# Optimization experiments

Measured on AMD Instinct MI355X. Metric: run time of the kernel, lower is better.

The kernel has to match this reference:

```python
import jax, jax.numpy as jnp
import numpy as np

N_NODES = 50000
N_EDGES = 800000
IN_CH, HID_CH, OUT_CH = 128, 256, 128


def _glorot(key, shape):
    fan_in, fan_out = shape[1], shape[0]
    lim = float(np.sqrt(6.0 / (fan_in + fan_out)))
    return jax.random.uniform(key, shape, jnp.float32, -lim, lim)


def setup_inputs() -> dict:
    key = jax.random.key(0)
    ks = jax.random.split(key, 8)
    x = jax.random.normal(ks[0], (N_NODES, IN_CH), jnp.float32)
    edge_index = jax.random.randint(ks[1], (2, N_EDGES), 0, N_NODES, jnp.int64)
    return {
        "x": x,
        "edge_index": edge_index,
        # layer 1: SAGEConv(128 -> 256): lin_l (with bias) on aggregated, lin_r (no bias) on root
        "W1l": _glorot(ks[2], (HID_CH, IN_CH)),
        "b1l": jnp.zeros((HID_CH,), jnp.float32),
        "W1r": _glorot(ks[3], (HID_CH, IN_CH)),
        # layer 2: SAGEConv(256 -> 128)
        "W2l": _glorot(ks[4], (OUT_CH, HID_CH)),
        "b2l": jnp.zeros((OUT_CH,), jnp.float32),
        "W2r": _glorot(ks[5], (OUT_CH, HID_CH)),
    }


def _sage_conv(x, src, dst, Wl, bl, Wr, n_nodes):
    # mean-aggregate neighbor (source) features at destination nodes
    msg = x[src]                                                   # [E, C] gather
    agg = jax.ops.segment_sum(msg, dst, num_segments=n_nodes)      # [N, C]
    deg = jax.ops.segment_sum(jnp.ones((src.shape[0],), x.dtype), dst,
                              num_segments=n_nodes)                # [N]
    mean = agg / jnp.maximum(deg, 1.0)[:, None]                    # zero-degree -> 0
    return mean @ Wl.T + bl + x @ Wr.T


def reference(x, edge_index, W1l, b1l, W1r, W2l, b2l, W2r):
    src, dst = edge_index[0], edge_index[1]
    n = x.shape[0]
    h = _sage_conv(x, src, dst, W1l, b1l, W1r, n)
    h = jax.nn.relu(h)  # dropout is identity in eval mode
    out = _sage_conv(h, src, dst, W2l, b2l, W2r, n)
    return out
```

## Files before the change

### kernel.cpp

```cpp
#include <hip/hip_runtime.h>

#define N_NODES 50000
#define IN_CH   128
#define HID_CH  256
#define OUT_CH  128

#define NB    196
#define NWG   256
#define NBNW  (NB * NWG)

#define XBLK  3125
#define WBLK  64

typedef __attribute__((ext_vector_type(8))) short bf16x8;
typedef __attribute__((ext_vector_type(4))) float f32x4;
typedef __attribute__((ext_vector_type(2))) float f32x2;

__device__ __forceinline__ unsigned short f32_bf16_rne(float f) {
    unsigned u = __float_as_uint(f);
    unsigned r = u + 0x7fff + ((u >> 16) & 1);
    return (unsigned short)(r >> 16);
}

__device__ __forceinline__ void cvt8_io(const float* __restrict__ inp,
                                        unsigned short* __restrict__ outp)
{
    const float4* p = reinterpret_cast<const float4*>(inp);
    float4 a = p[0], b = p[1];
    alignas(16) unsigned short t[8] = {
        f32_bf16_rne(a.x), f32_bf16_rne(a.y), f32_bf16_rne(a.z), f32_bf16_rne(a.w),
        f32_bf16_rne(b.x), f32_bf16_rne(b.y), f32_bf16_rne(b.z), f32_bf16_rne(b.w)};
    *reinterpret_cast<int4*>(outp) = *reinterpret_cast<const int4*>(t);
}

__global__ __launch_bounds__(256) void prep_kernel(
    const int* __restrict__ src, const int* __restrict__ dst,
    int* __restrict__ counts, int E, int chunk,
    const float* __restrict__ x, unsigned short* __restrict__ A1,
    unsigned char* __restrict__ xb8,
    const float* __restrict__ W1l, const float* __restrict__ W1r,
    const float* __restrict__ W2l, const float* __restrict__ W2r,
    unsigned short* __restrict__ B1, unsigned short* __restrict__ W2cat)
{
    const int b = blockIdx.x;
    if (b < NWG) {
        __shared__ int h[NB];
        for (int i = threadIdx.x; i < NB; i += 256) h[i] = 0;
        __syncthreads();
        const int e0 = b * chunk;
        const int e1 = min(e0 + chunk, E);
        for (int e = e0 + threadIdx.x; e < e1; e += 256) {
            int s = src[e], d = dst[e];
            if ((unsigned)s < (unsigned)N_NODES && (unsigned)d < (unsigned)N_NODES)
                atomicAdd(&h[d >> 8], 1);
        }
        __syncthreads();
        for (int i = threadIdx.x; i < NB; i += 256)
            counts[i * NWG + b] = h[i];
    } else if (b < NWG + XBLK) {
        size_t j = (size_t)(b - NWG) * 256 + threadIdx.x;
        const float4* p = reinterpret_cast<const float4*>(x) + 2 * j;
        float4 a = p[0], bb = p[1];
        alignas(16) unsigned short t[8] = {
            f32_bf16_rne(a.x),  f32_bf16_rne(a.y),  f32_bf16_rne(a.z),  f32_bf16_rne(a.w),
            f32_bf16_rne(bb.x), f32_bf16_rne(bb.y), f32_bf16_rne(bb.z), f32_bf16_rne(bb.w)};
        const size_t node = j >> 4, chunk16 = j & 15;
        *reinterpret_cast<int4*>(A1 + node * 256 + 128 + chunk16 * 8) =
            *reinterpret_cast<const int4*>(t);
        unsigned u0 = __builtin_amdgcn_cvt_pk_fp8_f32(a.x, a.y, 0, false);
        u0 = __builtin_amdgcn_cvt_pk_fp8_f32(a.z, a.w, u0, true);
        unsigned u1 = __builtin_amdgcn_cvt_pk_fp8_f32(bb.x, bb.y, 0, false);
        u1 = __builtin_amdgcn_cvt_pk_fp8_f32(bb.z, bb.w, u1, true);
        uint2 uv; uv.x = u0; uv.y = u1;
        *reinterpret_cast<uint2*>(xb8 + 8 * j) = uv;
    } else {
        int idx = (b - NWG - XBLK) * 256 + threadIdx.x;
        int seg = idx >> 12, j = idx & 4095;
        if (seg == 0) {
            int row = j >> 4, cb = (j & 15) * 8;
            cvt8_io(W1l + (size_t)j * 8, B1 + (size_t)row * 256 + cb);
        } else if (seg == 1) {
            int row = j >> 4, cb = (j & 15) * 8;
            cvt8_io(W1r + (size_t)j * 8, B1 + (size_t)row * 256 + 128 + cb);
        } else if (seg == 2) {
            int row = j >> 5, cb = (j & 31) * 8;
            cvt8_io(W2l + (size_t)j * 8, W2cat + (size_t)row * 256 + cb);
        } else {
            int row = j >> 5, cb = (j & 31) * 8;
            cvt8_io(W2r + (size_t)j * 8, W2cat + (size_t)(128 + row) * 256 + cb);
        }
    }
}

__global__ __launch_bounds__(256) void scan_kernel(
    const int* __restrict__ counts, int* __restrict__ S)
{
    __shared__ int red[256];
    const int t = threadIdx.x;
    const int b = blockIdx.x;
    const int lim = b * NWG;
    int partial = 0;
    for (int i = t; i < lim; i += 256) partial += counts[i];
    red[t] = partial;
    __syncthreads();
    for (int off = 128; off >= 1; off >>= 1) {
        if (t < off) red[t] += red[t + off];
        __syncthreads();
    }
    const int base_b = red[0];
    __syncthreads();
    const int v = counts[b * NWG + t];
    red[t] = v;
    __syncthreads();
    for (int off = 1; off < 256; off <<= 1) {
        int u = (t >= off) ? red[t - off] : 0;
        __syncthreads();
        if (t >= off) red[t] += u;
        __syncthreads();
    }
    S[b * NWG + t] = base_b + red[t] - v;
    if (b == NB - 1 && t == 255) S[NBNW] = base_b + red[255];
}

__global__ __launch_bounds__(256) void bscatter_kernel(
    const int* __restrict__ src, const int* __restrict__ dst,
    const int* __restrict__ S, int* __restrict__ pairs, int E, int chunk)
{
    __shared__ int cur[NB];
    const int w = blockIdx.x;
    for (int i = threadIdx.x; i < NB; i += 256) cur[i] = S[i * NWG + w];
    __syncthreads();
    const int e0 = w * chunk;
    const int e1 = min(e0 + chunk, E);
    for (int e = e0 + threadIdx.x; e < e1; e += 256) {
        int s = src[e], d = dst[e];
        if ((unsigned)s < (unsigned)N_NODES && (unsigned)d < (unsigned)N_NODES) {
            int pos = atomicAdd(&cur[d >> 8], 1);
            pairs[pos] = (s << 8) | (d & 255);
        }
    }
}

__global__ __launch_bounds__(256) void bsort_kernel(
    const int* __restrict__ pairs, const int* __restrict__ S,
    int* __restrict__ rowptr, int* __restrict__ colidx)
{
    __shared__ int hcnt[256];
    __shared__ int hcur[256];
    const int b = blockIdx.x;
    const int start = S[b * NWG];
    const int endv  = (b == NB - 1) ? S[NBNW] : S[(b + 1) * NWG];

    hcnt[threadIdx.x] = 0;
    __syncthreads();
    for (int e = start + threadIdx.x; e < endv; e += 256)
        atomicAdd(&hcnt[pairs[e] & 255], 1);
    __syncthreads();
    for (int off = 1; off < 256; off <<= 1) {
        int t = (threadIdx.x >= off) ? hcnt[threadIdx.x - off] : 0;
        __syncthreads();
        if (threadIdx.x >= off) hcnt[threadIdx.x] += t;
        __syncthreads();
    }
    int offv = (threadIdx.x == 0) ? 0 : hcnt[threadIdx.x - 1];
    hcur[threadIdx.x] = offv;
    int node = (b << 8) + threadIdx.x;
    if (node < N_NODES) rowptr[node] = start + offv;
    if (b == NB - 1 && threadIdx.x == 0) rowptr[N_NODES] = endv;
    __syncthreads();
    for (int e = start + threadIdx.x; e < endv; e += 256) {
        int p = pairs[e];
        int pos = atomicAdd(&hcur[p & 255], 1);
        colidx[start + pos] = (unsigned)p >> 8;
    }
}

#define ACC8(v)                                                              \
    { f32x2 t0 = __builtin_amdgcn_cvt_pk_f32_fp8(v.x, false);                \
      f32x2 t1 = __builtin_amdgcn_cvt_pk_f32_fp8(v.x, true);                 \
      f32x2 t2 = __builtin_amdgcn_cvt_pk_f32_fp8(v.y, false);                \
      f32x2 t3 = __builtin_amdgcn_cvt_pk_f32_fp8(v.y, true);                 \
      acc[0] += t0.x; acc[1] += t0.y; acc[2] += t1.x; acc[3] += t1.y;        \
      acc[4] += t2.x; acc[5] += t2.y; acc[6] += t3.x; acc[7] += t3.y; }

#define LDROW(s, CH) (*reinterpret_cast<const uint2*>(feat + (size_t)(s) * (CH) + l8 * 8))

#define AGG_BODY(CH)                                                            \
    const int node = blockIdx.x * 16 + (threadIdx.x >> 4);                      \
    if (node >= N_NODES) return;                                                \
    const int l8 = threadIdx.x & 15;                                            \
    const int beg = rowptr[node], end = rowptr[node + 1];                       \
    const int len = end - beg;                                                  \
    float acc[8] = {};                                                          \
    for (int base = beg; base < end; base += 16) {                              \
        const int cnt = min(16, end - base);                                    \
        int ci = colidx[base + ((l8 < cnt) ? l8 : 0)];                          \
        int k = 0;                                                              \
        for (; k + 7 < cnt; k += 8) {                                           \
            int s0 = __shfl(ci, k, 16),     s1 = __shfl(ci, k + 1, 16);         \
            int s2 = __shfl(ci, k + 2, 16), s3 = __shfl(ci, k + 3, 16);         \
            int s4 = __shfl(ci, k + 4, 16), s5 = __shfl(ci, k + 5, 16);         \
            int s6 = __shfl(ci, k + 6, 16), s7 = __shfl(ci, k + 7, 16);         \
            uint2 v0 = LDROW(s0, CH); uint2 v1 = LDROW(s1, CH);                 \
            uint2 v2 = LDROW(s2, CH); uint2 v3 = LDROW(s3, CH);                 \
            uint2 v4 = LDROW(s4, CH); uint2 v5 = LDROW(s5, CH);                 \
            uint2 v6 = LDROW(s6, CH); uint2 v7 = LDROW(s7, CH);                 \
            ACC8(v0) ACC8(v1) ACC8(v2) ACC8(v3)                                 \
            ACC8(v4) ACC8(v5) ACC8(v6) ACC8(v7)                                 \
        }                                                                       \
        for (; k + 3 < cnt; k += 4) {                                           \
            int s0 = __shfl(ci, k, 16),     s1 = __shfl(ci, k + 1, 16);         \
            int s2 = __shfl(ci, k + 2, 16), s3 = __shfl(ci, k + 3, 16);         \
            uint2 v0 = LDROW(s0, CH); uint2 v1 = LDROW(s1, CH);                 \
            uint2 v2 = LDROW(s2, CH); uint2 v3 = LDROW(s3, CH);                 \
            ACC8(v0) ACC8(v1) ACC8(v2) ACC8(v3)                                 \
        }                                                                       \
        for (; k < cnt; ++k) {                                                  \
            int s0 = __shfl(ci, k, 16);                                         \
            uint2 v0 = LDROW(s0, CH);                                           \
            ACC8(v0)                                                            \
        }                                                                       \
    }                                                                           \
    const float sc = 1.0f / fmaxf((float)len, 1.0f);

__global__ __launch_bounds__(256) void agg1_kernel(
    const unsigned char* __restrict__ feat, const int* __restrict__ rowptr,
    const int* __restrict__ colidx, unsigned short* __restrict__ A1)
{
    AGG_BODY(IN_CH)
    alignas(16) unsigned short t[8];
#pragma unroll
    for (int k = 0; k < 8; ++k) t[k] = f32_bf16_rne(acc[k] * sc);
    *reinterpret_cast<int4*>(A1 + (size_t)node * 256 + l8 * 8) =
        *reinterpret_cast<const int4*>(t);
}

__global__ __launch_bounds__(256) void agg2_kernel(
    const unsigned char* __restrict__ feat, const int* __restrict__ rowptr,
    const int* __restrict__ colidx, const unsigned short* __restrict__ hrb,
    const float* __restrict__ b2l, float* __restrict__ out)
{
    AGG_BODY(OUT_CH)
    const int4 hv = *reinterpret_cast<const int4*>(hrb + (size_t)node * OUT_CH + l8 * 8);
    const unsigned short* hs = reinterpret_cast<const unsigned short*>(&hv);
    float4 b0 = *reinterpret_cast<const float4*>(b2l + l8 * 8);
    float4 b1 = *reinterpret_cast<const float4*>(b2l + l8 * 8 + 4);
    float4 o0, o1;
    o0.x = acc[0] * sc + __uint_as_float((unsigned)hs[0] << 16) + b0.x;
    o0.y = acc[1] * sc + __uint_as_float((unsigned)hs[1] << 16) + b0.y;
    o0.z = acc[2] * sc + __uint_as_float((unsigned)hs[2] << 16) + b0.z;
    o0.w = acc[3] * sc + __uint_as_float((unsigned)hs[3] << 16) + b0.w;
    o1.x = acc[4] * sc + __uint_as_float((unsigned)hs[4] << 16) + b1.x;
    o1.y = acc[5] * sc + __uint_as_float((unsigned)hs[5] << 16) + b1.y;
    o1.z = acc[6] * sc + __uint_as_float((unsigned)hs[6] << 16) + b1.z;
    o1.w = acc[7] * sc + __uint_as_float((unsigned)hs[7] << 16) + b1.w;
    float* o = out + (size_t)node * OUT_CH + l8 * 8;
    reinterpret_cast<float4*>(o)[0] = o0;
    reinterpret_cast<float4*>(o)[1] = o1;
}

template <int NIT>
__device__ __forceinline__ void stage8(
    const unsigned short* __restrict__ g, int ldg, int rowBase, int maxRow,
    int kBase, unsigned short* __restrict__ s, int tid)
{
    const int wave = tid >> 6;
    const int lane = tid & 63;
    const int r_in = lane >> 3;
    const int c_g  = (lane & 7) ^ r_in;
#pragma unroll
    for (int it = 0; it < NIT; ++it) {
        const int rowBlk = it * 64 + wave * 8;
        int row = rowBase + rowBlk + r_in;
        if (row >= maxRow) row = maxRow - 1;
        const unsigned short* gp = g + (size_t)row * ldg + kBase + c_g * 8;
        unsigned short* lp = s + rowBlk * 64;
        __builtin_amdgcn_global_load_lds(
            (const __attribute__((address_space(1))) unsigned int*)gp,
            (__attribute__((address_space(3))) unsigned int*)lp,
            16, 0, 0);
    }
}

__device__ __forceinline__ const bf16x8* frag_ptr(
    const unsigned short* __restrict__ s, int rr, int c)
{
    return reinterpret_cast<const bf16x8*>(s + rr * 64 + (((c ^ (rr & 7))) << 3));
}

__device__ __forceinline__ void mfma_tile(
    const unsigned short* __restrict__ As, const unsigned short* __restrict__ Bs,
    int wm, int wn, int l16, int quad, f32x4 acc[4][4])
{
#pragma unroll
    for (int k0 = 0; k0 < 64; k0 += 32) {
        const int c = (k0 >> 3) + quad;
        bf16x8 a[4], b[4];
#pragma unroll
        for (int i = 0; i < 4; ++i)
            a[i] = *frag_ptr(As, wm * 64 + i * 16 + l16, c);
#pragma unroll
        for (int j = 0; j < 4; ++j)
            b[j] = *frag_ptr(Bs, wn * 64 + j * 16 + l16, c);
#pragma unroll
        for (int i = 0; i < 4; ++i)
#pragma unroll
            for (int j = 0; j < 4; ++j)
                acc[i][j] = __builtin_amdgcn_mfma_f32_16x16x32_bf16(
                    b[j], a[i], acc[i][j], 0, 0, 0);
    }
}

__global__ __launch_bounds__(512) void gemm1_mfma(
    const unsigned short* __restrict__ A1, const unsigned short* __restrict__ B1,
    const float* __restrict__ b1l, unsigned short* __restrict__ hb)
{
    __shared__ unsigned short As[128 * 64];
    __shared__ unsigned short Bs[256 * 64];
    const int tid = threadIdx.x;
    const int wid = tid >> 6, lane = tid & 63;
    const int wm = wid & 1, wn = wid >> 1;
    const int l16 = lane & 15, quad = lane >> 4;
    const int rowBase = blockIdx.x * 128;

    f32x4 z = {0.f, 0.f, 0.f, 0.f};
    f32x4 acc[4][4];
#pragma unroll
    for (int i = 0; i < 4; ++i)
#pragma unroll
        for (int j = 0; j < 4; ++j) acc[i][j] = z;

#pragma unroll
    for (int kb = 0; kb < 256; kb += 64) {
        __syncthreads();
        stage8<2>(A1, 256, rowBase, N_NODES, kb, As, tid);
        stage8<4>(B1, 256, 0, HID_CH, kb, Bs, tid);
        __syncthreads();
        mfma_tile(As, Bs, wm, wn, l16, quad, acc);
    }

#pragma unroll
    for (int i = 0; i < 4; ++i) {
        int m = rowBase + wm * 64 + i * 16 + l16;
        if (m >= N_NODES) continue;
#pragma unroll
        for (int j = 0; j < 4; ++j) {
            int col = wn * 64 + j * 16 + quad * 4;
            float4 bv = *reinterpret_cast<const float4*>(b1l + col);
            alignas(8) unsigned short t[4];
            t[0] = f32_bf16_rne(fmaxf(acc[i][j][0] + bv.x, 0.0f));
            t[1] = f32_bf16_rne(fmaxf(acc[i][j][1] + bv.y, 0.0f));
            t[2] = f32_bf16_rne(fmaxf(acc[i][j][2] + bv.z, 0.0f));
            t[3] = f32_bf16_rne(fmaxf(acc[i][j][3] + bv.w, 0.0f));
            *reinterpret_cast<uint2*>(hb + (size_t)m * HID_CH + col) =
                *reinterpret_cast<const uint2*>(t);
        }
    }
}

__global__ __launch_bounds__(512) void gemm2_mfma(
    const unsigned short* __restrict__ hb, const unsigned short* __restrict__ W2cat,
    unsigned char* __restrict__ pb8, unsigned short* __restrict__ hrb)
{
    __shared__ unsigned short As[128 * 64];
    __shared__ unsigned short Bs[256 * 64];
    const int tid = threadIdx.x;
    const int wid = tid >> 6, lane = tid & 63;
    const int wm = wid & 1, wn = wid >> 1;
    const int l16 = lane & 15, quad = lane >> 4;
    const int rowBase = blockIdx.x * 128;

    f32x4 z = {0.f, 0.f, 0.f, 0.f};
    f32x4 acc[4][4];
#pragma unroll
    for (int i = 0; i < 4; ++i)
#pragma unroll
        for (int j = 0; j < 4; ++j) acc[i][j] = z;

#pragma unroll
    for (int kb = 0; kb < HID_CH; kb += 64) {
        __syncthreads();
        stage8<2>(hb, HID_CH, rowBase, N_NODES, kb, As, tid);
        stage8<4>(W2cat, HID_CH, 0, 256, kb, Bs, tid);
        __syncthreads();
        mfma_tile(As, Bs, wm, wn, l16, quad, acc);
    }

    if (wn < 2) {
#pragma unroll
        for (int i = 0; i < 4; ++i) {
            int m = rowBase + wm * 64 + i * 16 + l16;
            if (m >= N_NODES) continue;
#pragma unroll
            for (int j = 0; j < 4; ++j) {
                int col = wn * 64 + j * 16 + quad * 4;
                unsigned u = __builtin_amdgcn_cvt_pk_fp8_f32(
                    acc[i][j][0], acc[i][j][1], 0, false);
                u = __builtin_amdgcn_cvt_pk_fp8_f32(
                    acc[i][j][2], acc[i][j][3], u, true);
                *reinterpret_cast<unsigned*>(pb8 + (size_t)m * OUT_CH + col) = u;
            }
        }
    } else {
#pragma unroll
        for (int i = 0; i < 4; ++i) {
            int m = rowBase + wm * 64 + i * 16 + l16;
            if (m >= N_NODES) continue;
#pragma unroll
            for (int j = 0; j < 4; ++j) {
                int col = wn * 64 + j * 16 + quad * 4 - 128;
                alignas(8) unsigned short t[4];
                t[0] = f32_bf16_rne(acc[i][j][0]);
                t[1] = f32_bf16_rne(acc[i][j][1]);
                t[2] = f32_bf16_rne(acc[i][j][2]);
                t[3] = f32_bf16_rne(acc[i][j][3]);
                *reinterpret_cast<uint2*>(hrb + (size_t)m * OUT_CH + col) =
                    *reinterpret_cast<const uint2*>(t);
            }
        }
    }
}

extern "C" void kernel_launch(void* const* d_in, const int* in_sizes, int n_in,
                              void* d_out, int out_size, void* d_ws, size_t ws_size,
                              hipStream_t stream)
{
    const float* x   = (const float*)d_in[0];
    const int*   ei  = (const int*)d_in[1];
    const float* W1l = (const float*)d_in[2];
    const float* b1l = (const float*)d_in[3];
    const float* W1r = (const float*)d_in[4];
    const float* W2l = (const float*)d_in[5];
    const float* b2l = (const float*)d_in[6];
    const float* W2r = (const float*)d_in[7];

    const int E = in_sizes[1] / 2;
    const int* src = ei;
    const int* dst = ei + E;

    char* ws = (char*)d_ws;
    size_t off = 0;
    auto alloc = [&](size_t bytes) {
        void* p = ws + off;
        off += (bytes + 255) & ~(size_t)255;
        return p;
    };
    unsigned short* A1     = (unsigned short*)alloc((size_t)N_NODES * 256 * 2);
    unsigned char*  xb8    = (unsigned char*)alloc((size_t)N_NODES * IN_CH);
    unsigned short* hb     = (unsigned short*)alloc((size_t)N_NODES * HID_CH * 2);
    unsigned char*  pb8    = (unsigned char*)alloc((size_t)N_NODES * OUT_CH);
    unsigned short* hrb    = (unsigned short*)alloc((size_t)N_NODES * OUT_CH * 2);
    unsigned short* B1     = (unsigned short*)alloc((size_t)HID_CH * 256 * 2);
    unsigned short* W2cat  = (unsigned short*)alloc((size_t)256 * HID_CH * 2);
    int* counts = (int*)alloc((size_t)NBNW * 4);
    int* S      = (int*)alloc((size_t)(NBNW + 1) * 4);
    int* pairs  = (int*)alloc((size_t)E * 4);
    int* rowptr = (int*)alloc((size_t)(N_NODES + 1) * 4);
    int* colidx = (int*)alloc((size_t)E * 4);
    float* out = (float*)d_out;

    const int chunk = (E + NWG - 1) / NWG;

    prep_kernel<<<NWG + XBLK + WBLK, 256, 0, stream>>>(
        src, dst, counts, E, chunk, x, A1, xb8,
        W1l, W1r, W2l, W2r, B1, W2cat);
    scan_kernel<<<NB, 256, 0, stream>>>(counts, S);
    bscatter_kernel<<<NWG, 256, 0, stream>>>(src, dst, S, pairs, E, chunk);
    bsort_kernel<<<NB, 256, 0, stream>>>(pairs, S, rowptr, colidx);

    const int aggBlocks = (N_NODES + 15) / 16;
    const int mBlocks = (N_NODES + 127) / 128;

    agg1_kernel<<<aggBlocks, 256, 0, stream>>>(xb8, rowptr, colidx, A1);
    gemm1_mfma<<<mBlocks, 512, 0, stream>>>(A1, B1, b1l, hb);
    gemm2_mfma<<<mBlocks, 512, 0, stream>>>(hb, W2cat, pb8, hrb);
    agg2_kernel<<<aggBlocks, 256, 0, stream>>>(pb8, rowptr, colidx, hrb, b2l, out);
}
```

Before: 213.9 us.

## Fuse layer-1 and layer-2 GEMMs, keeping the hidden tile in LDS

Merges gemm1 and gemm2 into one kernel. Each block's 128x256 bf16 hidden tile (bias plus ReLU applied) is written to a swizzled LDS buffer instead of global memory, and the second GEMM reads its A operand straight from LDS. This drops the global write and re-read of the full hidden activation and one kernel launch. The cost is about 112KB of LDS per block, which cuts occupancy to one block per CU and may serialise the grid into more waves.

```diff
diff --git a/kernel.cpp b/kernel.cpp
--- a/kernel.cpp
+++ b/kernel.cpp
@@ -288,6 +288,13 @@
     return reinterpret_cast<const bf16x8*>(s + rr * 64 + (((c ^ (rr & 7))) << 3));
 }
 
+__device__ __forceinline__ const bf16x8* hfrag_ptr(
+    const unsigned short* __restrict__ s, int rr, int kbc, int c)
+{
+    return reinterpret_cast<const bf16x8*>(
+        s + rr * 256 + ((kbc + (c ^ (rr & 7))) << 3));
+}
+
 __device__ __forceinline__ void mfma_tile(
     const unsigned short* __restrict__ As, const unsigned short* __restrict__ Bs,
     int wm, int wn, int l16, int quad, f32x4 acc[4][4])
@@ -311,12 +318,37 @@
     }
 }
 
-__global__ __launch_bounds__(512) void gemm1_mfma(
+__device__ __forceinline__ void mfma_tile_h(
+    const unsigned short* __restrict__ Hs, const unsigned short* __restrict__ Bs,
+    int kbc, int wm, int wn, int l16, int quad, f32x4 acc[4][4])
+{
+#pragma unroll
+    for (int k0 = 0; k0 < 64; k0 += 32) {
+        const int c = (k0 >> 3) + quad;
+        bf16x8 a[4], b[4];
+#pragma unroll
+        for (int i = 0; i < 4; ++i)
+            a[i] = *hfrag_ptr(Hs, wm * 64 + i * 16 + l16, kbc, c);
+#pragma unroll
+        for (int j = 0; j < 4; ++j)
+            b[j] = *frag_ptr(Bs, wn * 64 + j * 16 + l16, c);
+#pragma unroll
+        for (int i = 0; i < 4; ++i)
+#pragma unroll
+            for (int j = 0; j < 4; ++j)
+                acc[i][j] = __builtin_amdgcn_mfma_f32_16x16x32_bf16(
+                    b[j], a[i], acc[i][j], 0, 0, 0);
+    }
+}
+
+__global__ __launch_bounds__(512) void gemm_fused(
     const unsigned short* __restrict__ A1, const unsigned short* __restrict__ B1,
-    const float* __restrict__ b1l, unsigned short* __restrict__ hb)
+    const float* __restrict__ b1l, const unsigned short* __restrict__ W2cat,
+    unsigned char* __restrict__ pb8, unsigned short* __restrict__ hrb)
 {
     __shared__ unsigned short As[128 * 64];
     __shared__ unsigned short Bs[256 * 64];
+    __shared__ unsigned short Hs[128 * 256];
     const int tid = threadIdx.x;
     const int wid = tid >> 6, lane = tid & 63;
     const int wm = wid & 1, wn = wid >> 1;
@@ -341,37 +373,25 @@
 
 #pragma unroll
     for (int i = 0; i < 4; ++i) {
-        int m = rowBase + wm * 64 + i * 16 + l16;
-        if (m >= N_NODES) continue;
+        const int rr = wm * 64 + i * 16 + l16;
 #pragma unroll
         for (int j = 0; j < 4; ++j) {
-            int col = wn * 64 + j * 16 + quad * 4;
-            float4 bv = *reinterpret_cast<const float4*>(b1l + col);
+            const int colBase = wn * 64 + j * 16 + quad * 4;
+            float4 bv = *reinterpret_cast<const float4*>(b1l + colBase);
             alignas(8) unsigned short t[4];
             t[0] = f32_bf16_rne(fmaxf(acc[i][j][0] + bv.x, 0.0f));
             t[1] = f32_bf16_rne(fmaxf(acc[i][j][1] + bv.y, 0.0f));
             t[2] = f32_bf16_rne(fmaxf(acc[i][j][2] + bv.z, 0.0f));
             t[3] = f32_bf16_rne(fmaxf(acc[i][j][3] + bv.w, 0.0f));
-            *reinterpret_cast<uint2*>(hb + (size_t)m * HID_CH + col) =
-                *reinterpret_cast<const uint2*>(t);
-        }
-    }
-}
-
-__global__ __launch_bounds__(512) void gemm2_mfma(
-    const unsigned short* __restrict__ hb, const unsigned short* __restrict__ W2cat,
-    unsigned char* __restrict__ pb8, unsigned short* __restrict__ hrb)
-{
-    __shared__ unsigned short As[128 * 64];
-    __shared__ unsigned short Bs[256 * 64];
-    const int tid = threadIdx.x;
-    const int wid = tid >> 6, lane = tid & 63;
-    const int wm = wid & 1, wn = wid >> 1;
-    const int l16 = lane & 15, quad = lane >> 4;
-    const int rowBase = blockIdx.x * 128;
-
-    f32x4 z = {0.f, 0.f, 0.f, 0.f};
-    f32x4 acc[4][4];
+            const int grp  = colBase >> 6;
+            const int lc   = (colBase >> 3) & 7;
+            const int half = (colBase >> 2) & 1;
+            unsigned short* hp = Hs + rr * 256 +
+                (((grp << 3) + (lc ^ (rr & 7))) << 3) + half * 4;
+            *reinterpret_cast<uint2*>(hp) = *reinterpret_cast<const uint2*>(t);
+        }
+    }
+
 #pragma unroll
     for (int i = 0; i < 4; ++i)
 #pragma unroll
@@ -380,10 +400,9 @@
 #pragma unroll
     for (int kb = 0; kb < HID_CH; kb += 64) {
         __syncthreads();
-        stage8<2>(hb, HID_CH, rowBase, N_NODES, kb, As, tid);
         stage8<4>(W2cat, HID_CH, 0, 256, kb, Bs, tid);
         __syncthreads();
-        mfma_tile(As, Bs, wm, wn, l16, quad, acc);
+        mfma_tile_h(Hs, Bs, kb >> 3, wm, wn, l16, quad, acc);
     }
 
     if (wn < 2) {
@@ -447,7 +466,6 @@
     };
     unsigned short* A1     = (unsigned short*)alloc((size_t)N_NODES * 256 * 2);
     unsigned char*  xb8    = (unsigned char*)alloc((size_t)N_NODES * IN_CH);
-    unsigned short* hb     = (unsigned short*)alloc((size_t)N_NODES * HID_CH * 2);
     unsigned char*  pb8    = (unsigned char*)alloc((size_t)N_NODES * OUT_CH);
     unsigned short* hrb    = (unsigned short*)alloc((size_t)N_NODES * OUT_CH * 2);
     unsigned short* B1     = (unsigned short*)alloc((size_t)HID_CH * 256 * 2);
@@ -472,7 +490,6 @@
     const int mBlocks = (N_NODES + 127) / 128;
 
     agg1_kernel<<<aggBlocks, 256, 0, stream>>>(xb8, rowptr, colidx, A1);
-    gemm1_mfma<<<mBlocks, 512, 0, stream>>>(A1, B1, b1l, hb);
-    gemm2_mfma<<<mBlocks, 512, 0, stream>>>(hb, W2cat, pb8, hrb);
+    gemm_fused<<<mBlocks, 512, 0, stream>>>(A1, B1, b1l, W2cat, pb8, hrb);
     agg2_kernel<<<aggBlocks, 256, 0, stream>>>(pb8, rowptr, colidx, hrb, b2l, out);
 }
```

Result: no change. 211.6 us (-1.1%).
